# Optimization experiments

Hardware: AMD Instinct MI355X
Metric: run time of the kernel (lower is better)

## Reference

```python
import jax, jax.numpy as jnp
import numpy as np

D_MODEL = 1024
N_HEADS = 16
HEAD_DIM = D_MODEL // N_HEADS


def setup_inputs() -> dict:
    key = jax.random.key(0)
    ks = jax.random.split(key, 5)
    B, T = 4, 4096
    x = jax.random.normal(ks[0], (B, T, D_MODEL), dtype=jnp.float32)
    s = 1.0 / np.sqrt(D_MODEL)
    Wqkv = jax.random.normal(ks[1], (D_MODEL, 3 * D_MODEL), dtype=jnp.float32) * s
    bqkv = jnp.zeros((3 * D_MODEL,), dtype=jnp.float32)
    Wout = jax.random.normal(ks[2], (D_MODEL, D_MODEL), dtype=jnp.float32) * s
    bout = jnp.zeros((D_MODEL,), dtype=jnp.float32)
    return {"x": x, "Wqkv": Wqkv, "bqkv": bqkv, "Wout": Wout, "bout": bout}


def _feature_map(x):
    # elu(x) + 1  (strictly positive feature map)
    return jax.nn.elu(x) + 1.0


def reference(x, Wqkv, bqkv, Wout, bout):
    B, T, C = x.shape
    H, D = N_HEADS, HEAD_DIM
    qkv = x @ Wqkv + bqkv                      # [B,T,3C]
    qkv = qkv.reshape(B, T, 3, H, D)
    qkv = jnp.transpose(qkv, (2, 0, 3, 1, 4))  # [3,B,H,T,D]
    q, k, v = qkv[0], qkv[1], qkv[2]
    scale = D ** 0.25
    q_m = _feature_map(q / scale)
    k_m = _feature_map(k / scale)
    kv = jnp.einsum('bhtd,bhtm->bhdm', k_m, v)     # [B,H,D,D]
    out = jnp.einsum('bhtd,bhdm->bhtm', q_m, kv)   # [B,H,T,D]
    z = q_m.sum(axis=-1, keepdims=True)            # note: sum over feature dim (as in source)
    out = out / (z + 1e-6)
    out = jnp.transpose(out, (0, 2, 1, 3)).reshape(B, T, C)
    return out @ Wout + bout
```

## Files before the change

### kernel.cpp

```cpp
#include <hip/hip_runtime.h>
#include <hip/hip_bf16.h>
#include <math.h>

#define B_ 4
#define T_ 4096
#define H_ 16
#define D_ 64
#define C_ 1024
#define BT_ (B_*T_)

using short8  = __attribute__((ext_vector_type(8))) short;
using floatx4 = __attribute__((ext_vector_type(4))) float;

__device__ __forceinline__ float feature_map(float x) {
    return x > 0.0f ? x + 1.0f : __expf(x);
}
__device__ __forceinline__ unsigned short f2bf(float x) {
    union { __hip_bfloat16 b; unsigned short u; } c;
    c.b = __float2bfloat16(x);
    return c.u;
}
__device__ __forceinline__ float bf2f(unsigned short u) {
    union { unsigned int u; float f; } c;
    c.u = (unsigned)u << 16;
    return c.f;
}
__device__ __forceinline__ void async16(const void* g, void* l) {
    __builtin_amdgcn_global_load_lds(
        (const __attribute__((address_space(1))) void*)g,
        (__attribute__((address_space(3))) void*)l, 16, 0, 0);
}

__global__ __launch_bounds__(256)
void convert_x_kernel(const float4* __restrict__ x, ushort* __restrict__ xb)
{
    const size_t i = (size_t)blockIdx.x * 256 + threadIdx.x;
    const float4 v = x[i];
    *reinterpret_cast<ushort4*>(&xb[i * 4]) =
        make_ushort4(f2bf(v.x), f2bf(v.y), f2bf(v.z), f2bf(v.w));
}

__global__ __launch_bounds__(256)
void transpose_bf16_kernel(const float* __restrict__ W, ushort* __restrict__ WT,
                           int K, int N)
{
    __shared__ float t[32][33];
    const int n0 = blockIdx.x * 32, k0 = blockIdx.y * 32;
    const int r = threadIdx.x >> 5, c = threadIdx.x & 31;
    #pragma unroll
    for (int i = 0; i < 4; i++)
        t[r + 8 * i][c] = W[(size_t)(k0 + r + 8 * i) * N + n0 + c];
    __syncthreads();
    #pragma unroll
    for (int i = 0; i < 4; i++)
        WT[(size_t)(n0 + r + 8 * i) * K + k0 + c] = f2bf(t[c][r + 8 * i]);
}

__global__ __launch_bounds__(256)
void kv_mfma_kernel(const ushort* __restrict__ xb, const ushort* __restrict__ WqkvT,
                    const float* __restrict__ bqkv, float* __restrict__ kv)
{
    __shared__ __align__(16) unsigned char smem[34816];
    ushort* As = (ushort*)smem;
    ushort* Bs = (ushort*)(smem + 8192);
    ushort* kT = (ushort*)smem;
    ushort* vT = kT + 64 * 136;

    const int tid = threadIdx.x;
    const int w = tid >> 6, l = tid & 63;
    const int wm = w >> 1, wn = w & 1;
    const int lr = l & 15, quad = l >> 4;
    const int lk8 = quad * 8;
    const int h = blockIdx.x;
    const int mBase = blockIdx.y * 128;
    const int bb = mBase >> 12;

    const int srow = w * 32 + (l >> 2);
    const int scol = (l & 3) * 8;
    const ushort* gA = xb + (size_t)(mBase + srow) * C_ + scol;
    const int br0 = (srow < 64)      ? (C_ + h * 64 + srow)      : (2 * C_ + h * 64 + srow - 64);
    const int br1 = (srow + 16 < 64) ? (C_ + h * 64 + srow + 16) : (2 * C_ + h * 64 + srow - 48);
    const ushort* gB0 = WqkvT + (size_t)br0 * C_ + scol;
    const ushort* gB1 = WqkvT + (size_t)br1 * C_ + scol;
    void* ldsA = (void*)(smem + w * 2048);
    void* ldsB = (void*)(smem + 8192 + w * 2048);

    floatx4 acc[4][4];
    #pragma unroll
    for (int i = 0; i < 4; i++)
        #pragma unroll
        for (int j = 0; j < 4; j++) acc[i][j] = (floatx4)0.0f;

    for (int k0 = 0; k0 < C_; k0 += 32) {
        __syncthreads();
        async16(gA + k0, ldsA);
        async16(gA + 16 * C_ + k0, (void*)((char*)ldsA + 1024));
        async16(gB0 + k0, ldsB);
        async16(gB1 + k0, (void*)((char*)ldsB + 1024));
        __syncthreads();

        short8 af[4], bf[4];
        #pragma unroll
        for (int mt = 0; mt < 4; mt++)
            af[mt] = *(const short8*)&As[(wm * 64 + mt * 16 + lr) * 32 + lk8];
        #pragma unroll
        for (int nt = 0; nt < 4; nt++)
            bf[nt] = *(const short8*)&Bs[(wn * 64 + nt * 16 + lr) * 32 + lk8];
        #pragma unroll
        for (int mt = 0; mt < 4; mt++)
            #pragma unroll
            for (int nt = 0; nt < 4; nt++)
                acc[mt][nt] = __builtin_amdgcn_mfma_f32_16x16x32_bf16(
                    af[mt], bf[nt], acc[mt][nt], 0, 0, 0);
    }

    const float inv_scale = 0.35355339059327373f;
    const int bbias = (wn ? 2 * C_ : C_) + h * 64;

    __syncthreads();
    {
        ushort* dst = wn ? vT : kT;
        #pragma unroll
        for (int nt = 0; nt < 4; nt++) {
            const int cc = nt * 16 + lr;
            const float bv = bqkv[bbias + cc];
            #pragma unroll
            for (int mt = 0; mt < 4; mt++) {
                float v0 = acc[mt][nt][0] + bv, v1 = acc[mt][nt][1] + bv;
                float v2 = acc[mt][nt][2] + bv, v3 = acc[mt][nt][3] + bv;
                if (wn == 0) {
                    v0 = feature_map(v0 * inv_scale); v1 = feature_map(v1 * inv_scale);
                    v2 = feature_map(v2 * inv_scale); v3 = feature_map(v3 * inv_scale);
                }
                *(ushort4*)&dst[cc * 136 + wm * 64 + mt * 16 + quad * 4] =
                    make_ushort4(f2bf(v0), f2bf(v1), f2bf(v2), f2bf(v3));
            }
        }
    }
    __syncthreads();

    floatx4 acc2[2][2];
    #pragma unroll
    for (int i = 0; i < 2; i++)
        #pragma unroll
        for (int j = 0; j < 2; j++) acc2[i][j] = (floatx4)0.0f;

    #pragma unroll
    for (int kst = 0; kst < 4; kst++) {
        short8 afr[2], bfr[2];
        #pragma unroll
        for (int i = 0; i < 2; i++)
            afr[i] = *(const short8*)&kT[(wm * 32 + i * 16 + lr) * 136 + kst * 32 + lk8];
        #pragma unroll
        for (int j = 0; j < 2; j++)
            bfr[j] = *(const short8*)&vT[(wn * 32 + j * 16 + lr) * 136 + kst * 32 + lk8];
        #pragma unroll
        for (int i = 0; i < 2; i++)
            #pragma unroll
            for (int j = 0; j < 2; j++)
                acc2[i][j] = __builtin_amdgcn_mfma_f32_16x16x32_bf16(
                    afr[i], bfr[j], acc2[i][j], 0, 0, 0);
    }

    float* kvb = kv + (size_t)(bb * H_ + h) * (D_ * D_);
    #pragma unroll
    for (int i = 0; i < 2; i++)
        #pragma unroll
        for (int j = 0; j < 2; j++)
            #pragma unroll
            for (int r = 0; r < 4; r++) {
                const int d = wm * 32 + i * 16 + quad * 4 + r;
                const int m = wn * 32 + j * 16 + lr;
                atomicAdd(&kvb[d * 64 + m], acc2[i][j][r]);
            }
}

__global__ __launch_bounds__(256)
void qattn_mfma_kernel(const ushort* __restrict__ xb, const ushort* __restrict__ WqkvT,
                       const float* __restrict__ bqkv, const float* __restrict__ kv,
                       ushort* __restrict__ attn)
{
    __shared__ __align__(16) unsigned char smem[54272];
    ushort* As  = (ushort*)smem;
    ushort* Bs  = (ushort*)(smem + 8192);
    ushort* qS  = (ushort*)smem;
    ushort* kvT = (ushort*)(smem + 34816);
    float*  zS  = (float*)(smem + 53248);

    const int tid = threadIdx.x;
    const int w = tid >> 6, l = tid & 63;
    const int wm = w >> 1, wn = w & 1;
    const int lr = l & 15, quad = l >> 4;
    const int lk8 = quad * 8;
    const int hp = blockIdx.x;
    const int mBase = blockIdx.y * 128;
    const int bb = mBase >> 12;

    {
        const float* kvg = kv + ((size_t)bb * H_ + hp * 2) * (D_ * D_);
        #pragma unroll
        for (int e = 0; e < 32; e++) {
            const int flat = e * 256 + tid;
            const int hh = flat >> 12, d = (flat >> 6) & 63, m = flat & 63;
            kvT[hh * 4608 + m * 72 + d] = f2bf(kvg[flat]);
        }
    }

    const int srow = w * 32 + (l >> 2);
    const int scol = (l & 3) * 8;
    const ushort* gA = xb + (size_t)(mBase + srow) * C_ + scol;
    const ushort* gB = WqkvT + (size_t)(hp * 128 + srow) * C_ + scol;
    void* ldsA = (void*)(smem + w * 2048);
    void* ldsB = (void*)(smem + 8192 + w * 2048);

    floatx4 acc[4][4];
    #pragma unroll
    for (int i = 0; i < 4; i++)
        #pragma unroll
        for (int j = 0; j < 4; j++) acc[i][j] = (floatx4)0.0f;

    for (int k0 = 0; k0 < C_; k0 += 32) {
        __syncthreads();
        async16(gA + k0, ldsA);
        async16(gA + 16 * C_ + k0, (void*)((char*)ldsA + 1024));
        async16(gB + k0, ldsB);
        async16(gB + 16 * C_ + k0, (void*)((char*)ldsB + 1024));
        __syncthreads();

        short8 af[4], bfr[4];
        #pragma unroll
        for (int mt = 0; mt < 4; mt++)
            af[mt] = *(const short8*)&As[(wm * 64 + mt * 16 + lr) * 32 + lk8];
        #pragma unroll
        for (int nt = 0; nt < 4; nt++)
            bfr[nt] = *(const short8*)&Bs[(wn * 64 + nt * 16 + lr) * 32 + lk8];
        #pragma unroll
        for (int mt = 0; mt < 4; mt++)
            #pragma unroll
            for (int nt = 0; nt < 4; nt++)
                acc[mt][nt] = __builtin_amdgcn_mfma_f32_16x16x32_bf16(
                    af[mt], bfr[nt], acc[mt][nt], 0, 0, 0);
    }

    const float inv_scale = 0.35355339059327373f;

    __syncthreads();
    #pragma unroll
    for (int nt = 0; nt < 4; nt++) {
        const int cc = wn * 64 + nt * 16 + lr;
        const float bv = bqkv[hp * 128 + cc];
        #pragma unroll
        for (int mt = 0; mt < 4; mt++)
            #pragma unroll
            for (int i = 0; i < 4; i++) {
                const int t = wm * 64 + mt * 16 + quad * 4 + i;
                qS[t * 136 + cc] = f2bf(feature_map((acc[mt][nt][i] + bv) * inv_scale));
            }
    }
    __syncthreads();

    {
        const int t = tid & 127, hh = tid >> 7;
        float s = 0.0f;
        #pragma unroll
        for (int c8 = 0; c8 < 8; c8++) {
            const short8 v = *(const short8*)&qS[t * 136 + hh * 64 + c8 * 8];
            #pragma unroll
            for (int j = 0; j < 8; j++) s += bf2f((unsigned short)v[j]);
        }
        zS[hh * 128 + t] = s;
    }

    floatx4 acc3[4][4];
    #pragma unroll
    for (int i = 0; i < 4; i++)
        #pragma unroll
        for (int j = 0; j < 4; j++) acc3[i][j] = (floatx4)0.0f;

    #pragma unroll
    for (int kst = 0; kst < 2; kst++) {
        short8 afr[4], bfr[4];
        #pragma unroll
        for (int mt = 0; mt < 4; mt++)
            afr[mt] = *(const short8*)&qS[(wm * 64 + mt * 16 + lr) * 136 + wn * 64 + kst * 32 + lk8];
        #pragma unroll
        for (int nt = 0; nt < 4; nt++)
            bfr[nt] = *(const short8*)&kvT[wn * 4608 + (nt * 16 + lr) * 72 + kst * 32 + lk8];
        #pragma unroll
        for (int mt = 0; mt < 4; mt++)
            #pragma unroll
            for (int nt = 0; nt < 4; nt++)
                acc3[mt][nt] = __builtin_amdgcn_mfma_f32_16x16x32_bf16(
                    afr[mt], bfr[nt], acc3[mt][nt], 0, 0, 0);
    }
    __syncthreads();

    #pragma unroll
    for (int mt = 0; mt < 4; mt++)
        #pragma unroll
        for (int i = 0; i < 4; i++) {
            const int t = wm * 64 + mt * 16 + quad * 4 + i;
            const float inv = 1.0f / (zS[wn * 128 + t] + 1e-6f);
            #pragma unroll
            for (int nt = 0; nt < 4; nt++)
                qS[t * 136 + wn * 64 + nt * 16 + lr] = f2bf(acc3[mt][nt][i] * inv);
        }
    __syncthreads();

    #pragma unroll
    for (int it = 0; it < 16; it++) {
        const int flat = it * 256 + tid;
        const int row = flat >> 5, c = flat & 31;
        *(ushort4*)&attn[(size_t)(mBase + row) * C_ + hp * 128 + c * 4] =
            *(const ushort4*)&qS[row * 136 + c * 4];
    }
}

__global__ __launch_bounds__(256)
void outproj_mfma_kernel(const ushort* __restrict__ attn, const ushort* __restrict__ WoutT,
                         const float* __restrict__ bout, float* __restrict__ out)
{
    __shared__ __align__(16) unsigned char smem[16384];
    ushort* As = (ushort*)smem;
    ushort* Bs = (ushort*)(smem + 8192);

    const int tid = threadIdx.x;
    const int w = tid >> 6, l = tid & 63;
    const int wm = w >> 1, wn = w & 1;
    const int lr = l & 15, lk8 = (l >> 4) * 8;
    const int mBase = blockIdx.y * 128;
    const int nBase = blockIdx.x * 128;

    const int srow = w * 32 + (l >> 2);
    const int scol = (l & 3) * 8;
    const ushort* gA = attn + (size_t)(mBase + srow) * C_ + scol;
    const ushort* gB = WoutT + (size_t)(nBase + srow) * C_ + scol;
    void* ldsA = (void*)(smem + w * 2048);
    void* ldsB = (void*)(smem + 8192 + w * 2048);

    floatx4 acc[4][4];
    #pragma unroll
    for (int i = 0; i < 4; i++)
        #pragma unroll
        for (int j = 0; j < 4; j++) acc[i][j] = (floatx4)0.0f;

    for (int k0 = 0; k0 < C_; k0 += 32) {
        __syncthreads();
        async16(gA + k0, ldsA);
        async16(gA + 16 * C_ + k0, (void*)((char*)ldsA + 1024));
        async16(gB + k0, ldsB);
        async16(gB + 16 * C_ + k0, (void*)((char*)ldsB + 1024));
        __syncthreads();

        short8 af[4], bfr[4];
        #pragma unroll
        for (int mt = 0; mt < 4; mt++)
            af[mt] = *(const short8*)&As[(wm * 64 + mt * 16 + lr) * 32 + lk8];
        #pragma unroll
        for (int nt = 0; nt < 4; nt++)
            bfr[nt] = *(const short8*)&Bs[(wn * 64 + nt * 16 + lr) * 32 + lk8];
        #pragma unroll
        for (int mt = 0; mt < 4; mt++)
            #pragma unroll
            for (int nt = 0; nt < 4; nt++)
                acc[mt][nt] = __builtin_amdgcn_mfma_f32_16x16x32_bf16(
                    af[mt], bfr[nt], acc[mt][nt], 0, 0, 0);
    }

    #pragma unroll
    for (int mt = 0; mt < 4; mt++)
        #pragma unroll
        for (int nt = 0; nt < 4; nt++) {
            const int cc = nBase + wn * 64 + nt * 16 + lr;
            const float bv = bout[cc];
            #pragma unroll
            for (int i = 0; i < 4; i++) {
                const int rr = mBase + wm * 64 + mt * 16 + (l >> 4) * 4 + i;
                out[(size_t)rr * C_ + cc] = acc[mt][nt][i] + bv;
            }
        }
}

extern "C" void kernel_launch(void* const* d_in, const int* in_sizes, int n_in,
                              void* d_out, int out_size, void* d_ws, size_t ws_size,
                              hipStream_t stream)
{
    const float* x    = (const float*)d_in[0];
    const float* Wqkv = (const float*)d_in[1];
    const float* bqkv = (const float*)d_in[2];
    const float* Wout = (const float*)d_in[3];
    const float* bout = (const float*)d_in[4];
    float* out = (float*)d_out;

    char* ws = (char*)d_ws;
    ushort* xb     = (ushort*)ws;
    ushort* WqkvT  = (ushort*)(ws + 33554432);
    ushort* WoutT  = (ushort*)(ws + 39845888);
    ushort* attn   = (ushort*)(ws + 41943040);
    float*  kv     = (float*) (ws + 75497472);

    hipMemsetAsync(kv, 0, (size_t)B_ * H_ * D_ * D_ * sizeof(float), stream);

    convert_x_kernel<<<(BT_ * C_ / 4) / 256, 256, 0, stream>>>((const float4*)x, xb);
    transpose_bf16_kernel<<<dim3(3 * C_ / 32, C_ / 32), 256, 0, stream>>>(Wqkv, WqkvT, C_, 3 * C_);
    transpose_bf16_kernel<<<dim3(C_ / 32, C_ / 32), 256, 0, stream>>>(Wout, WoutT, C_, C_);

    kv_mfma_kernel<<<dim3(H_, BT_ / 128), 256, 0, stream>>>(xb, WqkvT, bqkv, kv);
    qattn_mfma_kernel<<<dim3(H_ / 2, BT_ / 128), 256, 0, stream>>>(xb, WqkvT, bqkv, kv, attn);
    outproj_mfma_kernel<<<dim3(C_ / 128, BT_ / 128), 256, 0, stream>>>(attn, WoutT, bout, out);
}
```

Before: 350.6 us.

## Compute Q in the KV projection pass and apply kv in a light follow-up kernel

The KV kernel now projects Q, K and V together using a 128x192 tile and writes feature-mapped Q as bf16 to a per-head workspace. A new small pv_kernel loads that Q and the finished kv matrix, applies the normalisation and writes attn. The previous qattn kernel, which recomputed the Q projection GEMM by rereading x, is gone. The cost is one extra bf16 Q write and read, plus more accumulator registers in the main GEMM (4x6 tiles), which may lower occupancy. attn now reuses the xb buffer, which is safe because xb is no longer read after the first kernel.

```diff
diff --git a/kernel.cpp b/kernel.cpp
--- a/kernel.cpp
+++ b/kernel.cpp
@@ -57,14 +57,16 @@
 }
 
 __global__ __launch_bounds__(256)
-void kv_mfma_kernel(const ushort* __restrict__ xb, const ushort* __restrict__ WqkvT,
-                    const float* __restrict__ bqkv, float* __restrict__ kv)
+void qkv_kv_kernel(const ushort* __restrict__ xb, const ushort* __restrict__ WqkvT,
+                   const float* __restrict__ bqkv, float* __restrict__ kv,
+                   ushort* __restrict__ qws)
 {
     __shared__ __align__(16) unsigned char smem[34816];
     ushort* As = (ushort*)smem;
     ushort* Bs = (ushort*)(smem + 8192);
     ushort* kT = (ushort*)smem;
     ushort* vT = kT + 64 * 136;
+    ushort* qS = (ushort*)smem;
 
     const int tid = threadIdx.x;
     const int w = tid >> 6, l = tid & 63;
@@ -74,65 +76,74 @@
     const int h = blockIdx.x;
     const int mBase = blockIdx.y * 128;
     const int bb = mBase >> 12;
-
-    const int srow = w * 32 + (l >> 2);
-    const int scol = (l & 3) * 8;
-    const ushort* gA = xb + (size_t)(mBase + srow) * C_ + scol;
-    const int br0 = (srow < 64)      ? (C_ + h * 64 + srow)      : (2 * C_ + h * 64 + srow - 64);
-    const int br1 = (srow + 16 < 64) ? (C_ + h * 64 + srow + 16) : (2 * C_ + h * 64 + srow - 48);
-    const ushort* gB0 = WqkvT + (size_t)br0 * C_ + scol;
-    const ushort* gB1 = WqkvT + (size_t)br1 * C_ + scol;
+    const int tloc = mBase & (T_ - 1);
+
+    const int srowA = w * 32 + (l >> 2);
+    const int scolA = (l & 3) * 8;
+    const ushort* gA = xb + (size_t)(mBase + srowA) * C_ + scolA;
     void* ldsA = (void*)(smem + w * 2048);
-    void* ldsB = (void*)(smem + 8192 + w * 2048);
-
-    floatx4 acc[4][4];
+
+    const ushort* gB[3];
+    void* ldsB[3];
+    #pragma unroll
+    for (int i = 0; i < 3; i++) {
+        const int r = w * 48 + i * 16 + (l >> 2);
+        const int grow = (r < 64)  ? (C_ + h * 64 + r)
+                       : (r < 128) ? (2 * C_ + h * 64 + (r - 64))
+                                   : (h * 64 + (r - 128));
+        gB[i] = WqkvT + (size_t)grow * C_ + (l & 3) * 8;
+        ldsB[i] = (void*)(smem + 8192 + w * 3072 + i * 1024);
+    }
+
+    floatx4 acc[4][6];
     #pragma unroll
     for (int i = 0; i < 4; i++)
         #pragma unroll
-        for (int j = 0; j < 4; j++) acc[i][j] = (floatx4)0.0f;
+        for (int j = 0; j < 6; j++) acc[i][j] = (floatx4)0.0f;
 
     for (int k0 = 0; k0 < C_; k0 += 32) {
         __syncthreads();
         async16(gA + k0, ldsA);
         async16(gA + 16 * C_ + k0, (void*)((char*)ldsA + 1024));
-        async16(gB0 + k0, ldsB);
-        async16(gB1 + k0, (void*)((char*)ldsB + 1024));
+        #pragma unroll
+        for (int i = 0; i < 3; i++) async16(gB[i] + k0, ldsB[i]);
         __syncthreads();
 
-        short8 af[4], bf[4];
+        short8 af[4], bfr[6];
         #pragma unroll
         for (int mt = 0; mt < 4; mt++)
             af[mt] = *(const short8*)&As[(wm * 64 + mt * 16 + lr) * 32 + lk8];
         #pragma unroll
-        for (int nt = 0; nt < 4; nt++)
-            bf[nt] = *(const short8*)&Bs[(wn * 64 + nt * 16 + lr) * 32 + lk8];
-        #pragma unroll
-        for (int mt = 0; mt < 4; mt++)
-            #pragma unroll
-            for (int nt = 0; nt < 4; nt++)
+        for (int nt = 0; nt < 6; nt++)
+            bfr[nt] = *(const short8*)&Bs[(wn * 96 + nt * 16 + lr) * 32 + lk8];
+        #pragma unroll
+        for (int mt = 0; mt < 4; mt++)
+            #pragma unroll
+            for (int nt = 0; nt < 6; nt++)
                 acc[mt][nt] = __builtin_amdgcn_mfma_f32_16x16x32_bf16(
-                    af[mt], bf[nt], acc[mt][nt], 0, 0, 0);
+                    af[mt], bfr[nt], acc[mt][nt], 0, 0, 0);
     }
 
     const float inv_scale = 0.35355339059327373f;
-    const int bbias = (wn ? 2 * C_ : C_) + h * 64;
-
-    __syncthreads();
-    {
-        ushort* dst = wn ? vT : kT;
-        #pragma unroll
-        for (int nt = 0; nt < 4; nt++) {
-            const int cc = nt * 16 + lr;
-            const float bv = bqkv[bbias + cc];
+
+    __syncthreads();
+    #pragma unroll
+    for (int nt = 0; nt < 6; nt++) {
+        const int ct = wn * 6 + nt;
+        if (ct < 8) {
+            const bool isK = ct < 4;
+            const int dcol = (ct - (isK ? 0 : 4)) * 16 + lr;
+            const float bv = bqkv[(isK ? C_ : 2 * C_) + h * 64 + dcol];
+            ushort* dst = isK ? kT : vT;
             #pragma unroll
             for (int mt = 0; mt < 4; mt++) {
                 float v0 = acc[mt][nt][0] + bv, v1 = acc[mt][nt][1] + bv;
                 float v2 = acc[mt][nt][2] + bv, v3 = acc[mt][nt][3] + bv;
-                if (wn == 0) {
+                if (isK) {
                     v0 = feature_map(v0 * inv_scale); v1 = feature_map(v1 * inv_scale);
                     v2 = feature_map(v2 * inv_scale); v3 = feature_map(v3 * inv_scale);
                 }
-                *(ushort4*)&dst[cc * 136 + wm * 64 + mt * 16 + quad * 4] =
+                *(ushort4*)&dst[dcol * 136 + wm * 64 + mt * 16 + quad * 4] =
                     make_ushort4(f2bf(v0), f2bf(v1), f2bf(v2), f2bf(v3));
             }
         }
@@ -168,48 +179,151 @@
         #pragma unroll
         for (int j = 0; j < 2; j++)
             #pragma unroll
-            for (int r = 0; r < 4; r++) {
-                const int d = wm * 32 + i * 16 + quad * 4 + r;
-                const int m = wn * 32 + j * 16 + lr;
-                atomicAdd(&kvb[d * 64 + m], acc2[i][j][r]);
-            }
+            for (int r = 0; r < 4; r++)
+                atomicAdd(&kvb[(wm * 32 + i * 16 + quad * 4 + r) * 64 + wn * 32 + j * 16 + lr],
+                          acc2[i][j][r]);
+
+    __syncthreads();
+    if (wn == 1) {
+        #pragma unroll
+        for (int nt = 2; nt < 6; nt++) {
+            const int qc = (nt - 2) * 16 + lr;
+            const float bv = bqkv[h * 64 + qc];
+            #pragma unroll
+            for (int mt = 0; mt < 4; mt++)
+                #pragma unroll
+                for (int i = 0; i < 4; i++)
+                    qS[(wm * 64 + mt * 16 + quad * 4 + i) * 72 + qc] =
+                        f2bf(feature_map((acc[mt][nt][i] + bv) * inv_scale));
+        }
+    }
+    __syncthreads();
+
+    ushort* qdst = qws + ((size_t)(bb * H_ + h) * T_ + tloc) * 64;
+    #pragma unroll
+    for (int it = 0; it < 8; it++) {
+        const int flat = it * 256 + tid;
+        const int row = flat >> 4, c4 = flat & 15;
+        *(ushort4*)&qdst[(size_t)row * 64 + c4 * 4] =
+            *(const ushort4*)&qS[row * 72 + c4 * 4];
+    }
 }
 
 __global__ __launch_bounds__(256)
-void qattn_mfma_kernel(const ushort* __restrict__ xb, const ushort* __restrict__ WqkvT,
-                       const float* __restrict__ bqkv, const float* __restrict__ kv,
-                       ushort* __restrict__ attn)
-{
-    __shared__ __align__(16) unsigned char smem[54272];
-    ushort* As  = (ushort*)smem;
-    ushort* Bs  = (ushort*)(smem + 8192);
+void pv_kernel(const ushort* __restrict__ qws, const float* __restrict__ kv,
+               ushort* __restrict__ attn)
+{
+    __shared__ __align__(16) unsigned char smem[26112];
     ushort* qS  = (ushort*)smem;
-    ushort* kvT = (ushort*)(smem + 34816);
-    float*  zS  = (float*)(smem + 53248);
+    ushort* kvT = (ushort*)(smem + 16384);
+    float*  zS  = (float*)(smem + 25600);
+    ushort* oS  = (ushort*)smem;
 
     const int tid = threadIdx.x;
     const int w = tid >> 6, l = tid & 63;
     const int wm = w >> 1, wn = w & 1;
     const int lr = l & 15, quad = l >> 4;
     const int lk8 = quad * 8;
-    const int hp = blockIdx.x;
+    const int bh = blockIdx.x;
+    const int b = bh >> 4, h = bh & 15;
+    const int t0 = blockIdx.y * 128;
+
+    {
+        const int row8 = l >> 3, c8 = (l & 7) * 8;
+        const ushort* gq = qws + ((size_t)bh * T_ + t0) * 64;
+        #pragma unroll
+        for (int i = 0; i < 4; i++) {
+            const int rbase = (w * 4 + i) * 8;
+            async16(gq + (size_t)(rbase + row8) * 64 + c8,
+                    (void*)(smem + (w * 4 + i) * 1024));
+        }
+    }
+    {
+        const float* kvg = kv + (size_t)bh * (D_ * D_);
+        #pragma unroll
+        for (int e = 0; e < 16; e++) {
+            const int flat = e * 256 + tid;
+            const int d = flat >> 6, m = flat & 63;
+            kvT[m * 72 + d] = f2bf(kvg[flat]);
+        }
+    }
+    __syncthreads();
+
+    if (tid < 128) {
+        float s = 0.0f;
+        #pragma unroll
+        for (int c8 = 0; c8 < 8; c8++) {
+            const short8 v = *(const short8*)&qS[tid * 64 + c8 * 8];
+            #pragma unroll
+            for (int j = 0; j < 8; j++) s += bf2f((unsigned short)v[j]);
+        }
+        zS[tid] = s;
+    }
+
+    floatx4 acc[4][2];
+    #pragma unroll
+    for (int i = 0; i < 4; i++)
+        #pragma unroll
+        for (int j = 0; j < 2; j++) acc[i][j] = (floatx4)0.0f;
+
+    #pragma unroll
+    for (int kst = 0; kst < 2; kst++) {
+        short8 af[4], bf[2];
+        #pragma unroll
+        for (int mt = 0; mt < 4; mt++)
+            af[mt] = *(const short8*)&qS[(wm * 64 + mt * 16 + lr) * 64 + kst * 32 + lk8];
+        #pragma unroll
+        for (int nt = 0; nt < 2; nt++)
+            bf[nt] = *(const short8*)&kvT[(wn * 32 + nt * 16 + lr) * 72 + kst * 32 + lk8];
+        #pragma unroll
+        for (int mt = 0; mt < 4; mt++)
+            #pragma unroll
+            for (int nt = 0; nt < 2; nt++)
+                acc[mt][nt] = __builtin_amdgcn_mfma_f32_16x16x32_bf16(
+                    af[mt], bf[nt], acc[mt][nt], 0, 0, 0);
+    }
+    __syncthreads();
+
+    #pragma unroll
+    for (int mt = 0; mt < 4; mt++)
+        #pragma unroll
+        for (int i = 0; i < 4; i++) {
+            const int t = wm * 64 + mt * 16 + quad * 4 + i;
+            const float inv = 1.0f / (zS[t] + 1e-6f);
+            #pragma unroll
+            for (int nt = 0; nt < 2; nt++)
+                oS[t * 72 + wn * 32 + nt * 16 + lr] = f2bf(acc[mt][nt][i] * inv);
+        }
+    __syncthreads();
+
+    #pragma unroll
+    for (int it = 0; it < 8; it++) {
+        const int flat = it * 256 + tid;
+        const int row = flat >> 4, c4 = flat & 15;
+        *(ushort4*)&attn[(size_t)(b * T_ + t0 + row) * C_ + h * 64 + c4 * 4] =
+            *(const ushort4*)&oS[row * 72 + c4 * 4];
+    }
+}
+
+__global__ __launch_bounds__(256)
+void outproj_mfma_kernel(const ushort* __restrict__ attn, const ushort* __restrict__ WoutT,
+                         const float* __restrict__ bout, float* __restrict__ out)
+{
+    __shared__ __align__(16) unsigned char smem[16384];
+    ushort* As = (ushort*)smem;
+    ushort* Bs = (ushort*)(smem + 8192);
+
+    const int tid = threadIdx.x;
+    const int w = tid >> 6, l = tid & 63;
+    const int wm = w >> 1, wn = w & 1;
+    const int lr = l & 15, lk8 = (l >> 4) * 8;
     const int mBase = blockIdx.y * 128;
-    const int bb = mBase >> 12;
-
-    {
-        const float* kvg = kv + ((size_t)bb * H_ + hp * 2) * (D_ * D_);
-        #pragma unroll
-        for (int e = 0; e < 32; e++) {
-            const int flat = e * 256 + tid;
-            const int hh = flat >> 12, d = (flat >> 6) & 63, m = flat & 63;
-            kvT[hh * 4608 + m * 72 + d] = f2bf(kvg[flat]);
-        }
-    }
+    const int nBase = blockIdx.x * 128;
 
     const int srow = w * 32 + (l >> 2);
     const int scol = (l & 3) * 8;
-    const ushort* gA = xb + (size_t)(mBase + srow) * C_ + scol;
-    const ushort* gB = WqkvT + (size_t)(hp * 128 + srow) * C_ + scol;
+    const ushort* gA = attn + (size_t)(mBase + srow) * C_ + scol;
+    const ushort* gB = WoutT + (size_t)(nBase + srow) * C_ + scol;
     void* ldsA = (void*)(smem + w * 2048);
     void* ldsB = (void*)(smem + 8192 + w * 2048);
 
@@ -242,131 +356,6 @@
                     af[mt], bfr[nt], acc[mt][nt], 0, 0, 0);
     }
 
-    const float inv_scale = 0.35355339059327373f;
-
-    __syncthreads();
-    #pragma unroll
-    for (int nt = 0; nt < 4; nt++) {
-        const int cc = wn * 64 + nt * 16 + lr;
-        const float bv = bqkv[hp * 128 + cc];
-        #pragma unroll
-        for (int mt = 0; mt < 4; mt++)
-            #pragma unroll
-            for (int i = 0; i < 4; i++) {
-                const int t = wm * 64 + mt * 16 + quad * 4 + i;
-                qS[t * 136 + cc] = f2bf(feature_map((acc[mt][nt][i] + bv) * inv_scale));
-            }
-    }
-    __syncthreads();
-
-    {
-        const int t = tid & 127, hh = tid >> 7;
-        float s = 0.0f;
-        #pragma unroll
-        for (int c8 = 0; c8 < 8; c8++) {
-            const short8 v = *(const short8*)&qS[t * 136 + hh * 64 + c8 * 8];
-            #pragma unroll
-            for (int j = 0; j < 8; j++) s += bf2f((unsigned short)v[j]);
-        }
-        zS[hh * 128 + t] = s;
-    }
-
-    floatx4 acc3[4][4];
-    #pragma unroll
-    for (int i = 0; i < 4; i++)
-        #pragma unroll
-        for (int j = 0; j < 4; j++) acc3[i][j] = (floatx4)0.0f;
-
-    #pragma unroll
-    for (int kst = 0; kst < 2; kst++) {
-        short8 afr[4], bfr[4];
-        #pragma unroll
-        for (int mt = 0; mt < 4; mt++)
-            afr[mt] = *(const short8*)&qS[(wm * 64 + mt * 16 + lr) * 136 + wn * 64 + kst * 32 + lk8];
-        #pragma unroll
-        for (int nt = 0; nt < 4; nt++)
-            bfr[nt] = *(const short8*)&kvT[wn * 4608 + (nt * 16 + lr) * 72 + kst * 32 + lk8];
-        #pragma unroll
-        for (int mt = 0; mt < 4; mt++)
-            #pragma unroll
-            for (int nt = 0; nt < 4; nt++)
-                acc3[mt][nt] = __builtin_amdgcn_mfma_f32_16x16x32_bf16(
-                    afr[mt], bfr[nt], acc3[mt][nt], 0, 0, 0);
-    }
-    __syncthreads();
-
-    #pragma unroll
-    for (int mt = 0; mt < 4; mt++)
-        #pragma unroll
-        for (int i = 0; i < 4; i++) {
-            const int t = wm * 64 + mt * 16 + quad * 4 + i;
-            const float inv = 1.0f / (zS[wn * 128 + t] + 1e-6f);
-            #pragma unroll
-            for (int nt = 0; nt < 4; nt++)
-                qS[t * 136 + wn * 64 + nt * 16 + lr] = f2bf(acc3[mt][nt][i] * inv);
-        }
-    __syncthreads();
-
-    #pragma unroll
-    for (int it = 0; it < 16; it++) {
-        const int flat = it * 256 + tid;
-        const int row = flat >> 5, c = flat & 31;
-        *(ushort4*)&attn[(size_t)(mBase + row) * C_ + hp * 128 + c * 4] =
-            *(const ushort4*)&qS[row * 136 + c * 4];
-    }
-}
-
-__global__ __launch_bounds__(256)
-void outproj_mfma_kernel(const ushort* __restrict__ attn, const ushort* __restrict__ WoutT,
-                         const float* __restrict__ bout, float* __restrict__ out)
-{
-    __shared__ __align__(16) unsigned char smem[16384];
-    ushort* As = (ushort*)smem;
-    ushort* Bs = (ushort*)(smem + 8192);
-
-    const int tid = threadIdx.x;
-    const int w = tid >> 6, l = tid & 63;
-    const int wm = w >> 1, wn = w & 1;
-    const int lr = l & 15, lk8 = (l >> 4) * 8;
-    const int mBase = blockIdx.y * 128;
-    const int nBase = blockIdx.x * 128;
-
-    const int srow = w * 32 + (l >> 2);
-    const int scol = (l & 3) * 8;
-    const ushort* gA = attn + (size_t)(mBase + srow) * C_ + scol;
-    const ushort* gB = WoutT + (size_t)(nBase + srow) * C_ + scol;
-    void* ldsA = (void*)(smem + w * 2048);
-    void* ldsB = (void*)(smem + 8192 + w * 2048);
-
-    floatx4 acc[4][4];
-    #pragma unroll
-    for (int i = 0; i < 4; i++)
-        #pragma unroll
-        for (int j = 0; j < 4; j++) acc[i][j] = (floatx4)0.0f;
-
-    for (int k0 = 0; k0 < C_; k0 += 32) {
-        __syncthreads();
-        async16(gA + k0, ldsA);
-        async16(gA + 16 * C_ + k0, (void*)((char*)ldsA + 1024));
-        async16(gB + k0, ldsB);
-        async16(gB + 16 * C_ + k0, (void*)((char*)ldsB + 1024));
-        __syncthreads();
-
-        short8 af[4], bfr[4];
-        #pragma unroll
-        for (int mt = 0; mt < 4; mt++)
-            af[mt] = *(const short8*)&As[(wm * 64 + mt * 16 + lr) * 32 + lk8];
-        #pragma unroll
-        for (int nt = 0; nt < 4; nt++)
-            bfr[nt] = *(const short8*)&Bs[(wn * 64 + nt * 16 + lr) * 32 + lk8];
-        #pragma unroll
-        for (int mt = 0; mt < 4; mt++)
-            #pragma unroll
-            for (int nt = 0; nt < 4; nt++)
-                acc[mt][nt] = __builtin_amdgcn_mfma_f32_16x16x32_bf16(
-                    af[mt], bfr[nt], acc[mt][nt], 0, 0, 0);
-    }
-
     #pragma unroll
     for (int mt = 0; mt < 4; mt++)
         #pragma unroll
@@ -396,8 +385,9 @@
     ushort* xb     = (ushort*)ws;
     ushort* WqkvT  = (ushort*)(ws + 33554432);
     ushort* WoutT  = (ushort*)(ws + 39845888);
-    ushort* attn   = (ushort*)(ws + 41943040);
+    ushort* qws    = (ushort*)(ws + 41943040);
     float*  kv     = (float*) (ws + 75497472);
+    ushort* attn   = xb;
 
     hipMemsetAsync(kv, 0, (size_t)B_ * H_ * D_ * D_ * sizeof(float), stream);
 
@@ -405,7 +395,7 @@
     transpose_bf16_kernel<<<dim3(3 * C_ / 32, C_ / 32), 256, 0, stream>>>(Wqkv, WqkvT, C_, 3 * C_);
     transpose_bf16_kernel<<<dim3(C_ / 32, C_ / 32), 256, 0, stream>>>(Wout, WoutT, C_, C_);
 
-    kv_mfma_kernel<<<dim3(H_, BT_ / 128), 256, 0, stream>>>(xb, WqkvT, bqkv, kv);
-    qattn_mfma_kernel<<<dim3(H_ / 2, BT_ / 128), 256, 0, stream>>>(xb, WqkvT, bqkv, kv, attn);
+    qkv_kv_kernel<<<dim3(H_, BT_ / 128), 256, 0, stream>>>(xb, WqkvT, bqkv, kv, qws);
+    pv_kernel<<<dim3(B_ * H_, T_ / 128), 256, 0, stream>>>(qws, kv, attn);
     outproj_mfma_kernel<<<dim3(C_ / 128, BT_ / 128), 256, 0, stream>>>(attn, WoutT, bout, out);
 }
```

Result: slower. 468.7 us (+33.7%).
